# Performance work log

Measured on AMD Instinct MI355X. Metric: run time of the kernel, lower is better.

Reference implementation:

```python
import jax, jax.numpy as jnp
import numpy as np

N, M, D = 32768, 2048, 512
TOPK = 10  # top 5 -> pseudo-normal, next 5 -> pseudo-abnormal


def setup_inputs() -> dict:
    key = jax.random.key(0)
    k1, k2 = jax.random.split(key)
    query = jax.random.normal(k1, (N, D), dtype=jnp.float32)
    m = jax.random.uniform(k2, (M, D), dtype=jnp.float32)
    m_items = m / jnp.linalg.norm(m, axis=1, keepdims=True)  # F.normalize dim=1
    return {"query": query, "m_items": m_items}


def reference(query, m_items):
    # scores over memory, softmax along memory dim (dim=1)
    score = query @ m_items.T                      # [N, M]
    score_memory = jax.nn.softmax(score, axis=1)    # [N, M]

    # top-10 per row (descending); first 5 = top, next 5 = bottom
    top10_scores, top10_idx = jax.lax.top_k(score_memory, TOPK)
    top_scores, bot_scores = top10_scores[:, :5], top10_scores[:, 5:10]
    top_idx, bot_idx = top10_idx[:, :5], top10_idx[:, 5:10]

    # softmax over selected subsets (temperature = 1)
    w_top = jax.nn.softmax(top_scores, axis=1)      # [N, 5]
    w_bot = jax.nn.softmax(bot_scores, axis=1)      # [N, 5]

    top_keys = m_items[top_idx]                     # [N, 5, D]
    bot_keys = m_items[bot_idx]                     # [N, 5, D]

    top_output = jnp.einsum('nk,nkd->nd', w_top, top_keys)
    bot_output = jnp.einsum('nk,nkd->nd', w_bot, bot_keys)

    pseudo_normal = 0.5 * query + 0.5 * top_output
    pseudo_abnormal = 0.01 * query + 0.99 * bot_output
    return (pseudo_normal, pseudo_abnormal)
```

## Files before the change

### kernel.cpp

```cpp
#include <hip/hip_runtime.h>
#include <hip/hip_bf16.h>

#define NQ 32768
#define MI 2048
#define DD 512

typedef unsigned int u32;
typedef unsigned short u16;
typedef unsigned long long u64;

typedef __attribute__((ext_vector_type(8))) short bf16x8;
typedef __attribute__((ext_vector_type(4))) float f32x4;


__device__ __forceinline__ u16 f2bf_rne(float f) {
  u32 u = __builtin_bit_cast(u32, f);
  u += 0x7FFFu + ((u >> 16) & 1u);
  return (u16)(u >> 16);
}

__device__ __forceinline__ u16 f2h(float f) {
  return __builtin_bit_cast(u16, (_Float16)f);
}

__device__ __forceinline__ float h2f(u16 h) {
  return (float)__builtin_bit_cast(_Float16, h);
}

__device__ __forceinline__ void gload16(const void* g, void* l) {
  const __attribute__((address_space(1))) u32* gp =
      (const __attribute__((address_space(1))) u32*)g;
  __attribute__((address_space(3))) u32* lp =
      (__attribute__((address_space(3))) u32*)(u32)(size_t)l;
  __builtin_amdgcn_global_load_lds(gp, lp, 16, 0, 0);
}


__global__ __launch_bounds__(256) void cvt_kernel(const float* __restrict__ in,
                                                  u16* __restrict__ out, int n8) {
  int stride = gridDim.x * blockDim.x;
  for (int i = blockIdx.x * blockDim.x + threadIdx.x; i < n8; i += stride) {
    const f32x4* p = (const f32x4*)in + (size_t)i * 2;
    f32x4 a = p[0], b = p[1];
    uint4 o;
    o.x = (u32)f2bf_rne(a[0]) | ((u32)f2bf_rne(a[1]) << 16);
    o.y = (u32)f2bf_rne(a[2]) | ((u32)f2bf_rne(a[3]) << 16);
    o.z = (u32)f2bf_rne(b[0]) | ((u32)f2bf_rne(b[1]) << 16);
    o.w = (u32)f2bf_rne(b[2]) | ((u32)f2bf_rne(b[3]) << 16);
    ((uint4*)out)[i] = o;
  }
}


__global__ __launch_bounds__(256) void gemm_kernel(const u16* __restrict__ Qb,
                                                   const u16* __restrict__ Mb,
                                                   u32* __restrict__ SP) {
  __shared__ u16 As[128 * 64];
  __shared__ u16 Bs[128 * 64];
  const int t = threadIdx.x;
  const int l = t & 63, w = t >> 6;
  const int wr = w >> 1, wc = w & 1;
  const int bid = blockIdx.x;
  const int nb = (bid & 7) * 512 + (bid >> 3);
  const int bm = nb >> 4, bn = nb & 15;

  f32x4 acc[4][4] = {};
  const int l15 = l & 15, lg = l >> 4;

  const u16* Ag = Qb + (size_t)(bm * 128 + (t >> 3)) * DD + (t & 7) * 8;
  const u16* Bg = Mb + (size_t)(bn * 128 + (t >> 3)) * DD + (t & 7) * 8;
  char* Asl = (char*)As + t * 16;
  char* Bsl = (char*)Bs + t * 16;

  for (int kt = 0; kt < DD; kt += 64) {
#pragma unroll
    for (int i = 0; i < 4; ++i) {
      gload16(Ag + (size_t)i * 32 * DD + kt, Asl + i * 4096);
      gload16(Bg + (size_t)i * 32 * DD + kt, Bsl + i * 4096);
    }
    __syncthreads();
#pragma unroll
    for (int ks = 0; ks < 2; ++ks) {
      const int kk = ks * 32 + lg * 8;
      bf16x8 af[4], bfr[4];
#pragma unroll
      for (int mi = 0; mi < 4; ++mi)
        af[mi] = *(const bf16x8*)&As[(wr * 64 + mi * 16 + l15) * 64 + kk];
#pragma unroll
      for (int ni = 0; ni < 4; ++ni)
        bfr[ni] = *(const bf16x8*)&Bs[(wc * 64 + ni * 16 + l15) * 64 + kk];
#pragma unroll
      for (int mi = 0; mi < 4; ++mi)
#pragma unroll
        for (int ni = 0; ni < 4; ++ni)
          acc[mi][ni] = __builtin_amdgcn_mfma_f32_16x16x32_bf16(
              af[mi], bfr[ni], acc[mi][ni], 0, 0, 0);
    }
    __syncthreads();
  }

  const int r0 = bm * 128 + wr * 64 + (l >> 4) * 4;
  const int c0 = bn * 128 + wc * 64 + l15;
  const int p0 = r0 >> 1;
#pragma unroll
  for (int mi = 0; mi < 4; ++mi)
#pragma unroll
    for (int ni = 0; ni < 4; ++ni) {
      u32 lo = (u32)f2h(acc[mi][ni][0]) | ((u32)f2h(acc[mi][ni][1]) << 16);
      u32 hi = (u32)f2h(acc[mi][ni][2]) | ((u32)f2h(acc[mi][ni][3]) << 16);
      size_t base = (size_t)(p0 + mi * 8) * MI + (c0 + ni * 16);
      SP[base] = lo;
      SP[base + MI] = hi;
    }
}


#define MAX8T(b) fmaxf(fmaxf(fmaxf(k[b], k[b + 1]), fmaxf(k[b + 2], k[b + 3])), \
                       fmaxf(fmaxf(k[b + 4], k[b + 5]), fmaxf(k[b + 6], k[b + 7])))

#define REMOVE_GRP(b, gvar)                                   \
  {                                                           \
    _Pragma("unroll") for (int j = 0; j < 8; ++j)             \
        k[b + j] = (k[b + j] == gmax) ? -3e38f : k[b + j];    \
    gvar = MAX8T(b);                                          \
  }

__global__ __launch_bounds__(256) void finish_kernel(const float* __restrict__ q,
                                                     const float* __restrict__ m_items,
                                                     const u32* __restrict__ SP,
                                                     float* __restrict__ out) {
  const int w = threadIdx.x >> 6, l = threadIdx.x & 63;
  const int n = blockIdx.x * 4 + w;
  const int p = n >> 1, h = n & 1;

  const uint4* Sr = (const uint4*)(SP + (size_t)p * MI);
  float k[32];
#pragma unroll
  for (int i = 0; i < 8; ++i) {
    uint4 c = Sr[i * 64 + l];
    u32 wd[4] = {c.x, c.y, c.z, c.w};
#pragma unroll
    for (int j = 0; j < 4; ++j) {
      u16 hb = h ? (u16)(wd[j] >> 16) : (u16)(wd[j] & 0xFFFFu);
      float f = h2f(hb);
      int s = i * 4 + j;
      k[s] = __builtin_bit_cast(float,
                                (__builtin_bit_cast(u32, f) & ~31u) | (u32)(31 - s));
    }
  }

  float mx = k[0];
#pragma unroll
  for (int j = 1; j < 32; ++j) mx = fmaxf(mx, k[j]);
  for (int off = 32; off >= 1; off >>= 1) mx = fmaxf(mx, __shfl_xor(mx, off));
  float se = 0.f;
#pragma unroll
  for (int j = 0; j < 32; ++j) se += __expf(k[j] - mx);
  for (int off = 32; off >= 1; off >>= 1) se += __shfl_xor(se, off);
  const float invZ = 1.0f / se;

  float g0 = MAX8T(0), g1 = MAX8T(8), g2 = MAX8T(16), g3 = MAX8T(24);
  float pk = fmaxf(fmaxf(g0, g1), fmaxf(g2, g3));

  int mym = 0x7FFFFFFF;
  float mysc = -1e30f;
#pragma unroll 1
  for (int c = 0; c < 16; ++c) {
    float gmax = pk;
    for (int off = 32; off >= 1; off >>= 1) gmax = fmaxf(gmax, __shfl_xor(gmax, off));
    u32 gb = __builtin_bit_cast(u32, gmax);
    int jw = 31 - (int)(gb & 31u);
    u64 bal = __ballot(pk == gmax);
    int wl = (int)__ffsll(bal) - 1;
    int mwin = ((jw >> 2) << 8) + wl * 4 + (jw & 3);
    if (l == c) mym = mwin;
    int grp = __builtin_amdgcn_readfirstlane(jw >> 3);
    switch (grp) {
      case 0: REMOVE_GRP(0, g0); break;
      case 1: REMOVE_GRP(8, g1); break;
      case 2: REMOVE_GRP(16, g2); break;
      default: REMOVE_GRP(24, g3); break;
    }
    pk = fmaxf(fmaxf(g0, g1), fmaxf(g2, g3));
  }

  const f32x4* Q4 = (const f32x4*)(q + (size_t)n * DD);
  f32x4 q0 = Q4[l * 2], q1 = Q4[l * 2 + 1];
  for (int c = 0; c < 16; ++c) {
    int mc = __shfl(mym, c);
    const f32x4* M4 = (const f32x4*)(m_items + (size_t)mc * DD);
    f32x4 a = M4[l * 2], b = M4[l * 2 + 1];
    float pr = a[0] * q0[0] + a[1] * q0[1] + a[2] * q0[2] + a[3] * q0[3] +
               b[0] * q1[0] + b[1] * q1[1] + b[2] * q1[2] + b[3] * q1[3];
    for (int off = 32; off >= 1; off >>= 1) pr += __shfl_xor(pr, off);
    if (l == c) mysc = pr;
  }

  int rank = 0;
  for (int i = 0; i < 16; ++i) {
    float ov = __shfl(mysc, i);
    int om = __shfl(mym, i);
    rank += (ov > mysc || (ov == mysc && om < mym)) ? 1 : 0;
  }

  float prm = 0.f;
  int mr = 0;
  for (int r = 0; r < 10; ++r) {
    u64 bal = __ballot(rank == r);
    int sr = (int)__ffsll(bal) - 1;
    float sv = __shfl(mysc, sr);
    int sm = __shfl(mym, sr);
    float pv = __expf(sv - mx) * invZ;
    if (l == r) { prm = pv; mr = sm; }
  }

  f32x4 acc0a = q0 * 0.5f, acc0b = q1 * 0.5f;
  f32x4 acc1a = q0 * 0.01f, acc1b = q1 * 0.01f;

  float mt = -1e30f;
  for (int r = 0; r < 5; ++r) mt = fmaxf(mt, __shfl(prm, r));
  float Wt = 0.f;
  for (int r = 0; r < 5; ++r) Wt += __expf(__shfl(prm, r) - mt);
  float iWt = 0.5f / Wt;
  for (int r = 0; r < 5; ++r) {
    float pv = __shfl(prm, r);
    int mi = __shfl(mr, r);
    float wt = __expf(pv - mt) * iWt;
    const f32x4* M4 = (const f32x4*)(m_items + (size_t)mi * DD);
    acc0a += wt * M4[l * 2];
    acc0b += wt * M4[l * 2 + 1];
  }

  float mb = -1e30f;
  for (int r = 5; r < 10; ++r) mb = fmaxf(mb, __shfl(prm, r));
  float Wb = 0.f;
  for (int r = 5; r < 10; ++r) Wb += __expf(__shfl(prm, r) - mb);
  float iWb = 0.99f / Wb;
  for (int r = 5; r < 10; ++r) {
    float pv = __shfl(prm, r);
    int mi = __shfl(mr, r);
    float wt = __expf(pv - mb) * iWb;
    const f32x4* M4 = (const f32x4*)(m_items + (size_t)mi * DD);
    acc1a += wt * M4[l * 2];
    acc1b += wt * M4[l * 2 + 1];
  }

  f32x4* O0 = (f32x4*)(out + (size_t)n * DD);
  O0[l * 2] = acc0a;
  O0[l * 2 + 1] = acc0b;
  f32x4* O1 = (f32x4*)(out + (size_t)NQ * DD + (size_t)n * DD);
  O1[l * 2] = acc1a;
  O1[l * 2 + 1] = acc1b;
}


extern "C" void kernel_launch(void* const* d_in, const int* in_sizes, int n_in,
                              void* d_out, int out_size, void* d_ws, size_t ws_size,
                              hipStream_t stream) {
  const float* q = (const float*)d_in[0];
  const float* m = (const float*)d_in[1];
  float* out = (float*)d_out;

  u16* Qb = (u16*)d_ws;
  u16* Mb = Qb + (size_t)NQ * DD;
  u32* SP = (u32*)(Mb + (size_t)MI * DD);

  cvt_kernel<<<2048, 256, 0, stream>>>(q, Qb, NQ * DD / 8);
  cvt_kernel<<<512, 256, 0, stream>>>(m, Mb, MI * DD / 8);
  gemm_kernel<<<(NQ / 128) * (MI / 128), 256, 0, stream>>>(Qb, Mb, SP);
  finish_kernel<<<NQ / 4, 256, 0, stream>>>(q, m, SP, out);
}
```

Baseline: 426.8 us.

## Double-buffer GEMM LDS tiles and parallelize candidate rescoring across lane groups

The GEMM kernel now keeps two LDS buffers for the A and B tiles. It issues the global-to-LDS loads for the next K tile before running the MFMAs on the current one, which drops one barrier per iteration and overlaps memory with compute. In the top-k kernel, the 16 sequential wave-wide exact fp32 rescoring dot products are replaced by one pass where each group of 4 lanes computes one candidate's dot product, followed by a small shuffle reduction. This cuts the serial shuffle-reduction chains but doubles LDS use, which may lower occupancy, and the strided per-lane loads are less coalesced.

```diff
diff --git a/kernel.cpp b/kernel.cpp
--- a/kernel.cpp
+++ b/kernel.cpp
@@ -55,8 +55,8 @@
 __global__ __launch_bounds__(256) void gemm_kernel(const u16* __restrict__ Qb,
                                                    const u16* __restrict__ Mb,
                                                    u32* __restrict__ SP) {
-  __shared__ u16 As[128 * 64];
-  __shared__ u16 Bs[128 * 64];
+  __shared__ u16 As[2][128 * 64];
+  __shared__ u16 Bs[2][128 * 64];
   const int t = threadIdx.x;
   const int l = t & 63, w = t >> 6;
   const int wr = w >> 1, wc = w & 1;
@@ -69,26 +69,32 @@
 
   const u16* Ag = Qb + (size_t)(bm * 128 + (t >> 3)) * DD + (t & 7) * 8;
   const u16* Bg = Mb + (size_t)(bn * 128 + (t >> 3)) * DD + (t & 7) * 8;
-  char* Asl = (char*)As + t * 16;
-  char* Bsl = (char*)Bs + t * 16;
-
-  for (int kt = 0; kt < DD; kt += 64) {
-#pragma unroll
-    for (int i = 0; i < 4; ++i) {
-      gload16(Ag + (size_t)i * 32 * DD + kt, Asl + i * 4096);
-      gload16(Bg + (size_t)i * 32 * DD + kt, Bsl + i * 4096);
-    }
-    __syncthreads();
+
+#define STAGE(buf, kt)                                                      \
+  {                                                                         \
+    _Pragma("unroll") for (int i = 0; i < 4; ++i) {                         \
+      gload16(Ag + (size_t)i * 32 * DD + (kt), (char*)As[buf] + t * 16 + i * 4096); \
+      gload16(Bg + (size_t)i * 32 * DD + (kt), (char*)Bs[buf] + t * 16 + i * 4096); \
+    }                                                                       \
+  }
+
+  STAGE(0, 0);
+  __syncthreads();
+
+#pragma unroll
+  for (int t8 = 0; t8 < 8; ++t8) {
+    const int cur = t8 & 1;
+    if (t8 < 7) STAGE(cur ^ 1, (t8 + 1) * 64);
 #pragma unroll
     for (int ks = 0; ks < 2; ++ks) {
       const int kk = ks * 32 + lg * 8;
       bf16x8 af[4], bfr[4];
 #pragma unroll
       for (int mi = 0; mi < 4; ++mi)
-        af[mi] = *(const bf16x8*)&As[(wr * 64 + mi * 16 + l15) * 64 + kk];
+        af[mi] = *(const bf16x8*)&As[cur][(wr * 64 + mi * 16 + l15) * 64 + kk];
 #pragma unroll
       for (int ni = 0; ni < 4; ++ni)
-        bfr[ni] = *(const bf16x8*)&Bs[(wc * 64 + ni * 16 + l15) * 64 + kk];
+        bfr[ni] = *(const bf16x8*)&Bs[cur][(wc * 64 + ni * 16 + l15) * 64 + kk];
 #pragma unroll
       for (int mi = 0; mi < 4; ++mi)
 #pragma unroll
@@ -96,8 +102,9 @@
           acc[mi][ni] = __builtin_amdgcn_mfma_f32_16x16x32_bf16(
               af[mi], bfr[ni], acc[mi][ni], 0, 0, 0);
     }
-    __syncthreads();
-  }
+    if (t8 < 7) __syncthreads();
+  }
+#undef STAGE
 
   const int r0 = bm * 128 + wr * 64 + (l >> 4) * 4;
   const int c0 = bn * 128 + wc * 64 + l15;
@@ -163,7 +170,6 @@
   float pk = fmaxf(fmaxf(g0, g1), fmaxf(g2, g3));
 
   int mym = 0x7FFFFFFF;
-  float mysc = -1e30f;
 #pragma unroll 1
   for (int c = 0; c < 16; ++c) {
     float gmax = pk;
@@ -184,16 +190,19 @@
     pk = fmaxf(fmaxf(g0, g1), fmaxf(g2, g3));
   }
 
-  const f32x4* Q4 = (const f32x4*)(q + (size_t)n * DD);
-  f32x4 q0 = Q4[l * 2], q1 = Q4[l * 2 + 1];
-  for (int c = 0; c < 16; ++c) {
-    int mc = __shfl(mym, c);
-    const f32x4* M4 = (const f32x4*)(m_items + (size_t)mc * DD);
-    f32x4 a = M4[l * 2], b = M4[l * 2 + 1];
-    float pr = a[0] * q0[0] + a[1] * q0[1] + a[2] * q0[2] + a[3] * q0[3] +
-               b[0] * q1[0] + b[1] * q1[1] + b[2] * q1[2] + b[3] * q1[3];
-    for (int off = 32; off >= 1; off >>= 1) pr += __shfl_xor(pr, off);
-    if (l == c) mysc = pr;
+  const int mg = __shfl(mym, l >> 2);
+  float mysc;
+  {
+    const f32x4* Mr = (const f32x4*)(m_items + (size_t)mg * DD) + (l & 3) * 32;
+    const f32x4* Qr = (const f32x4*)(q + (size_t)n * DD) + (l & 3) * 32;
+    f32x4 ps = {0.f, 0.f, 0.f, 0.f};
+#pragma unroll
+    for (int j = 0; j < 32; ++j) ps += Mr[j] * Qr[j];
+    float s = ps[0] + ps[1] + ps[2] + ps[3];
+    s += __shfl_xor(s, 1);
+    s += __shfl_xor(s, 2);
+    float g = __shfl(s, (l & 15) * 4);
+    mysc = (l < 16) ? g : -1e30f;
   }
 
   int rank = 0;
@@ -206,7 +215,7 @@
   float prm = 0.f;
   int mr = 0;
   for (int r = 0; r < 10; ++r) {
-    u64 bal = __ballot(rank == r);
+    u64 bal = __ballot(rank == r && l < 16);
     int sr = (int)__ffsll(bal) - 1;
     float sv = __shfl(mysc, sr);
     int sm = __shfl(mym, sr);
@@ -214,6 +223,8 @@
     if (l == r) { prm = pv; mr = sm; }
   }
 
+  const f32x4* Q4 = (const f32x4*)(q + (size_t)n * DD);
+  f32x4 q0 = Q4[l * 2], q1 = Q4[l * 2 + 1];
   f32x4 acc0a = q0 * 0.5f, acc0b = q1 * 0.5f;
   f32x4 acc1a = q0 * 0.01f, acc1b = q1 * 0.01f;
 
```

Result: slower. 587.2 us (+37.6%).
